# Kernel optimization log

Measured on AMD Instinct MI355X. Metric: run time of the kernel, lower is better.

The kernel has to match this reference:

```python
import jax, jax.numpy as jnp
from jax import lax
import numpy as np

# CenterNet decode config
B, C, H, W = 16, 80, 128, 128  # batch, classes, feature-map H/W (512 input / down_ratio 4)
K = 100                        # top-K detections per image
DOWN = 4.0                     # down_ratio: feature-map coords -> input-image coords


def setup_inputs() -> dict:
    key = jax.random.key(0)
    k1, k2, k3 = jax.random.split(key, 3)
    return {
        "output_heatmap": jax.random.normal(k1, (B, C, H, W), dtype=jnp.float32),
        "output_bbox": jax.random.uniform(k2, (B, 2, H, W), dtype=jnp.float32) * 32.0,  # wh head
        "output_offset": jax.random.uniform(k3, (B, 2, H, W), dtype=jnp.float32),       # sub-pixel offset head
        "image_id": jnp.arange(B, dtype=jnp.int32),
    }


def reference(output_heatmap, output_bbox, output_offset, image_id):
    # 1) peak scores
    hm = jax.nn.sigmoid(output_heatmap)  # [B,C,H,W]
    # 2) 3x3 maxpool NMS: keep only local maxima
    hmax = lax.reduce_window(hm, -jnp.inf, lax.max,
                             window_dimensions=(1, 1, 3, 3),
                             window_strides=(1, 1, 1, 1),
                             padding='SAME')
    hm = jnp.where(hmax == hm, hm, jnp.zeros((), hm.dtype))
    # 3) per-image top-K over all classes and positions
    scores, inds = lax.top_k(hm.reshape(B, C * H * W), K)  # [B,K]
    cls = (inds // (H * W)).astype(jnp.float32)             # [B,K]
    sp = inds % (H * W)                                     # spatial index in [0, H*W)
    ys = (sp // W).astype(jnp.float32)
    xs = (sp % W).astype(jnp.float32)
    # 4) sparse gather of offset and wh at the K peak locations
    off = jnp.take_along_axis(output_offset.reshape(B, 2, H * W), sp[:, None, :], axis=2)  # [B,2,K]
    wh = jnp.take_along_axis(output_bbox.reshape(B, 2, H * W), sp[:, None, :], axis=2)     # [B,2,K]
    cx = xs + off[:, 0]
    cy = ys + off[:, 1]
    w = wh[:, 0]
    h = wh[:, 1]
    # 5) decode to corner boxes in input-image coordinates
    boxes = jnp.stack([cx - w / 2, cy - h / 2, cx + w / 2, cy + h / 2], axis=-1) * DOWN  # [B,K,4]
    img = jnp.broadcast_to(image_id[:, None].astype(jnp.float32), (B, K))
    # detections: [image_id, x1, y1, x2, y2, score, class] -> [B,K,7]
    det = jnp.concatenate([img[..., None], boxes, scores[..., None], cls[..., None]], axis=-1)
    return det
```

## Files before the change

kernel.cpp:

```cpp
#include <hip/hip_runtime.h>

#define BB 16
#define CC 80
#define HWs 16384
#define KK 100
#define NBIN 2048
#define BCAP 2304
#define SBCAP 128

#define OFF_BHIST 0
#define OFF_CUT   131072
#define OFF_PBCNT 131136
#define OFF_PSCNT 136256
#define OFF_REC   141376
#define OFF_SURV  11937856

__device__ __forceinline__ unsigned okey(float f) {
    unsigned u = __float_as_uint(f);
    return (u & 0x80000000u) ? ~u : (u | 0x80000000u);
}

__global__ __launch_bounds__(256) void zero_hist_kernel(int4* __restrict__ bhist) {
    int i = blockIdx.x * 256 + threadIdx.x;
    if (i < BB * NBIN / 4) bhist[i] = make_int4(0, 0, 0, 0);
}

__global__ __launch_bounds__(256) void nms_kernel(const float* __restrict__ hm,
                                                  unsigned* __restrict__ rec,
                                                  int* __restrict__ pbcnt,
                                                  int* __restrict__ bhist) {
    __shared__ int hist[NBIN];
    __shared__ unsigned sbuf[BCAP];
    __shared__ int s_n;
    const int plane = blockIdx.x;
    const int b = plane / CC;
    const int c = plane - b * CC;
    const int t = threadIdx.x;
    const int sx = t & 31;
    const int x0 = sx << 2;
    const int band0 = (t >> 5) << 4;
    const float4* __restrict__ src4 =
        reinterpret_cast<const float4*>(hm + (size_t)plane * HWs);

    for (int i = t; i < NBIN; i += 256) hist[i] = 0;
    if (t == 0) s_n = 0;
    __syncthreads();

    auto hmax3 = [&](const float4& a) -> float4 {
        float vm1 = __shfl_up(a.w, 1, 32);
        float vp4 = __shfl_down(a.x, 1, 32);
        if (sx == 0) vm1 = a.x;
        if (sx == 31) vp4 = a.w;
        float4 h;
        h.x = fmaxf(fmaxf(vm1, a.x), a.y);
        h.y = fmaxf(fmaxf(a.x, a.y), a.z);
        h.z = fmaxf(fmaxf(a.y, a.z), a.w);
        h.w = fmaxf(fmaxf(a.z, a.w), vp4);
        return h;
    };

#pragma unroll
    for (int chunk = 0; chunk < 2; ++chunk) {
        const int y0 = band0 + (chunk << 3);

        float4 w[10];
#pragma unroll
        for (int i = 0; i < 10; ++i) {
            int rr = y0 - 1 + i;
            rr = rr < 0 ? 0 : (rr > 127 ? 127 : rr);
            w[i] = src4[(rr << 5) + sx];
        }
        __builtin_amdgcn_sched_barrier(0);

        float4 hm1 = hmax3(w[0]);
        float4 h0  = hmax3(w[1]);
#pragma unroll
        for (int r = 0; r < 8; ++r) {
            float4 hp1 = hmax3(w[r + 2]);
            float vv[4] = { w[r + 1].x, w[r + 1].y, w[r + 1].z, w[r + 1].w };
            float mm[4] = { fmaxf(fmaxf(hm1.x, h0.x), hp1.x),
                            fmaxf(fmaxf(hm1.y, h0.y), hp1.y),
                            fmaxf(fmaxf(hm1.z, h0.z), hp1.z),
                            fmaxf(fmaxf(hm1.w, h0.w), hp1.w) };
#pragma unroll
            for (int j = 0; j < 4; ++j) {
                if (vv[j] >= mm[j]) {
                    int sl = atomicAdd(&s_n, 1);
                    unsigned bin = okey(vv[j]) >> 21;
                    unsigned idx = ((unsigned)c << 14)
                                 | ((unsigned)(y0 + r) << 7) | (unsigned)(x0 + j);
                    if (sl < BCAP) sbuf[sl] = (bin << 21) | idx;
                }
            }
            hm1 = h0; h0 = hp1;
        }
    }
    __syncthreads();
    int n = s_n; if (n > BCAP) n = BCAP;

    for (int i = t; i < n; i += 256) atomicAdd(&hist[sbuf[i] >> 21], 1);
    __syncthreads();
    for (int i = t; i < NBIN; i += 256) {
        int hv = hist[i];
        if (hv) atomicAdd(&bhist[b * NBIN + i], hv);
    }
    unsigned* __restrict__ rb = rec + (size_t)plane * BCAP;
    for (int i = t; i < n; i += 256) rb[i] = sbuf[i];
    if (t == 0) pbcnt[plane] = n;
}

__global__ __launch_bounds__(256) void cut_kernel(const int* __restrict__ bhist,
                                                  int* __restrict__ cut) {
    __shared__ int csum[256];
    __shared__ int s_cut;
    const int b = blockIdx.x;
    const int t = threadIdx.x;

    int h[8]; int chunk = 0;
#pragma unroll
    for (int j = 0; j < 8; ++j) {
        h[j] = bhist[b * NBIN + (t << 3) + j];
        chunk += h[j];
    }
    csum[t] = chunk;
    if (t == 0) s_cut = 0;
    __syncthreads();
    for (int off = 1; off < 256; off <<= 1) {
        int v = (t + off < 256) ? csum[t + off] : 0;
        __syncthreads();
        csum[t] += v;
        __syncthreads();
    }
    if (csum[0] > KK) {
        int running = (t < 255) ? csum[t + 1] : 0;
        if (csum[t] >= KK && running < KK) {
            for (int j = 7; j >= 0; --j) {
                running += h[j];
                if (running >= KK) { s_cut = (t << 3) + j; break; }
            }
        }
    }
    __syncthreads();
    if (t == 0) cut[b] = s_cut;
}

__global__ __launch_bounds__(256) void filter_kernel(const unsigned* __restrict__ rec,
                                                     const int* __restrict__ pbcnt,
                                                     const int* __restrict__ cut,
                                                     unsigned* __restrict__ surv,
                                                     int* __restrict__ pscnt) {
    __shared__ int s_n;
    const int bx = blockIdx.x;
    const int b = bx / CC;
    const int t = threadIdx.x;
    if (t == 0) s_n = 0;
    __syncthreads();

    int n = pbcnt[bx]; if (n > BCAP) n = BCAP;
    const int cutb = cut[b];
    const unsigned* __restrict__ rb = rec + (size_t)bx * BCAP;
    unsigned* __restrict__ sb = surv + (size_t)bx * SBCAP;
    for (int i = t; i < n; i += 256) {
        unsigned rv = rb[i];
        if ((int)(rv >> 21) >= cutb) {
            int sl = atomicAdd(&s_n, 1);
            if (sl < SBCAP) sb[sl] = rv & 0x1FFFFFu;
        }
    }
    __syncthreads();
    if (t == 0) pscnt[bx] = s_n > SBCAP ? SBCAP : s_n;
}

__global__ __launch_bounds__(256) void topk_kernel(const unsigned* __restrict__ surv,
                                                   const int* __restrict__ pscnt,
                                                   const float* __restrict__ hm,
                                                   const float* __restrict__ bbox,
                                                   const float* __restrict__ offs,
                                                   const int* __restrict__ image_id,
                                                   float* __restrict__ out) {
    __shared__ int lcnt[CC];
    __shared__ unsigned uidx[2048];
    __shared__ unsigned long long list[2048];
    __shared__ int s_n;
    const int b = blockIdx.x;
    const int t = threadIdx.x;
    const float* __restrict__ hb = hm + (size_t)b * CC * HWs;

    if (t < CC) lcnt[t] = pscnt[b * CC + t];
    if (t == 0) s_n = 0;
    __syncthreads();

    for (int s = t; s < CC; s += 256) {
        int cs = lcnt[s]; if (cs > SBCAP) cs = SBCAP;
        if (cs) {
            int base = atomicAdd(&s_n, cs);
            const unsigned* __restrict__ sb = surv + ((size_t)b * CC + s) * SBCAP;
            for (int k = 0; k < cs; ++k)
                if (base + k < 2048) uidx[base + k] = sb[k];
        }
    }
    __syncthreads();
    int n = s_n; if (n > 2048) n = 2048;

    for (int i = t; i < n; i += 256) {
        unsigned idx = uidx[i];
        float lv = hb[idx];
        float s = 1.0f / (1.0f + expf(-lv));
        list[i] = ((unsigned long long)__float_as_uint(s) << 32) | (unsigned)(~idx);
    }
    int P = 128;
    while (P < n) P <<= 1;
    for (int i = n + t; i < P; i += 256) list[i] = 0ull;
    __syncthreads();

    for (int ksz = 2; ksz <= P; ksz <<= 1) {
        for (int j = ksz >> 1; j > 0; j >>= 1) {
            for (int i = t; i < P; i += 256) {
                int ixj = i ^ j;
                if (ixj > i) {
                    unsigned long long a = list[i], bb2 = list[ixj];
                    bool desc = ((i & ksz) == 0);
                    if (desc ? (a < bb2) : (a > bb2)) { list[i] = bb2; list[ixj] = a; }
                }
            }
            __syncthreads();
        }
    }

    if (t < KK) {
        float s = 0.0f; unsigned idx = 0;
        if (t < n) {
            unsigned long long cv = list[t];
            s = __uint_as_float((unsigned)(cv >> 32));
            idx = ~(unsigned)(cv & 0xFFFFFFFFu) & 0x1FFFFFu;
        }
        unsigned sp = idx & (HWs - 1);
        float cls = (float)(idx >> 14);
        float ysf = (float)(sp >> 7);
        float xsf = (float)(sp & 127);
        const float* __restrict__ ob  = offs + (size_t)b * 2 * HWs;
        const float* __restrict__ bbx = bbox + (size_t)b * 2 * HWs;
        float cx = xsf + ob[sp];
        float cy = ysf + ob[HWs + sp];
        float w = bbx[sp];
        float h = bbx[HWs + sp];
        float* row = out + ((size_t)b * KK + t) * 7;
        row[0] = (float)image_id[b];
        row[1] = (cx - w * 0.5f) * 4.0f;
        row[2] = (cy - h * 0.5f) * 4.0f;
        row[3] = (cx + w * 0.5f) * 4.0f;
        row[4] = (cy + h * 0.5f) * 4.0f;
        row[5] = s;
        row[6] = cls;
    }
}

extern "C" void kernel_launch(void* const* d_in, const int* in_sizes, int n_in,
                              void* d_out, int out_size, void* d_ws, size_t ws_size,
                              hipStream_t stream) {
    const float* hm      = (const float*)d_in[0];
    const float* bbox    = (const float*)d_in[1];
    const float* offset  = (const float*)d_in[2];
    const int*   img_id  = (const int*)d_in[3];
    float* out = (float*)d_out;

    char* ws = (char*)d_ws;
    int*      bhist = (int*)(ws + OFF_BHIST);
    int*      cut   = (int*)(ws + OFF_CUT);
    int*      pbcnt = (int*)(ws + OFF_PBCNT);
    int*      pscnt = (int*)(ws + OFF_PSCNT);
    unsigned* rec   = (unsigned*)(ws + OFF_REC);
    unsigned* surv  = (unsigned*)(ws + OFF_SURV);

    zero_hist_kernel<<<32, 256, 0, stream>>>((int4*)bhist);
    nms_kernel<<<BB * CC, 256, 0, stream>>>(hm, rec, pbcnt, bhist);
    cut_kernel<<<BB, 256, 0, stream>>>(bhist, cut);
    filter_kernel<<<BB * CC, 256, 0, stream>>>(rec, pbcnt, cut, surv, pscnt);
    topk_kernel<<<BB, 256, 0, stream>>>(surv, pscnt, hm, bbox, offset, img_id, out);
}
```

Measured before the change: 62.75 us.

## Split NMS planes into half-plane blocks and fold cut computation into filter

Result: faster. 60.34 us (-3.8%).

```diff
diff --git a/kernel.cpp b/kernel.cpp
--- a/kernel.cpp
+++ b/kernel.cpp
@@ -5,15 +5,16 @@
 #define HWs 16384
 #define KK 100
 #define NBIN 2048
-#define BCAP 2304
-#define SBCAP 128
+#define NBLK (BB * CC * 2)
+#define NSLOT 160
+#define BCAP 1152
+#define SBCAP 64
 
 #define OFF_BHIST 0
-#define OFF_CUT   131072
-#define OFF_PBCNT 131136
-#define OFF_PSCNT 136256
-#define OFF_REC   141376
-#define OFF_SURV  11937856
+#define OFF_PBCNT 131072
+#define OFF_PSCNT 141312
+#define OFF_SURV  151552
+#define OFF_REC   806912
 
 __device__ __forceinline__ unsigned okey(float f) {
     unsigned u = __float_as_uint(f);
@@ -32,19 +33,30 @@
     __shared__ int hist[NBIN];
     __shared__ unsigned sbuf[BCAP];
     __shared__ int s_n;
-    const int plane = blockIdx.x;
+    const int blk = blockIdx.x;
+    const int plane = blk >> 1;
+    const int half = blk & 1;
     const int b = plane / CC;
     const int c = plane - b * CC;
     const int t = threadIdx.x;
     const int sx = t & 31;
     const int x0 = sx << 2;
-    const int band0 = (t >> 5) << 4;
+    const int y0 = (half << 6) + ((t >> 5) << 3);
     const float4* __restrict__ src4 =
         reinterpret_cast<const float4*>(hm + (size_t)plane * HWs);
 
     for (int i = t; i < NBIN; i += 256) hist[i] = 0;
     if (t == 0) s_n = 0;
     __syncthreads();
+
+    float4 w[10];
+#pragma unroll
+    for (int i = 0; i < 10; ++i) {
+        int rr = y0 - 1 + i;
+        rr = rr < 0 ? 0 : (rr > 127 ? 127 : rr);
+        w[i] = src4[(rr << 5) + sx];
+    }
+    __builtin_amdgcn_sched_barrier(0);
 
     auto hmax3 = [&](const float4& a) -> float4 {
         float vm1 = __shfl_up(a.w, 1, 32);
@@ -59,41 +71,27 @@
         return h;
     };
 
-#pragma unroll
-    for (int chunk = 0; chunk < 2; ++chunk) {
-        const int y0 = band0 + (chunk << 3);
-
-        float4 w[10];
-#pragma unroll
-        for (int i = 0; i < 10; ++i) {
-            int rr = y0 - 1 + i;
-            rr = rr < 0 ? 0 : (rr > 127 ? 127 : rr);
-            w[i] = src4[(rr << 5) + sx];
-        }
-        __builtin_amdgcn_sched_barrier(0);
-
-        float4 hm1 = hmax3(w[0]);
-        float4 h0  = hmax3(w[1]);
-#pragma unroll
-        for (int r = 0; r < 8; ++r) {
-            float4 hp1 = hmax3(w[r + 2]);
-            float vv[4] = { w[r + 1].x, w[r + 1].y, w[r + 1].z, w[r + 1].w };
-            float mm[4] = { fmaxf(fmaxf(hm1.x, h0.x), hp1.x),
-                            fmaxf(fmaxf(hm1.y, h0.y), hp1.y),
-                            fmaxf(fmaxf(hm1.z, h0.z), hp1.z),
-                            fmaxf(fmaxf(hm1.w, h0.w), hp1.w) };
-#pragma unroll
-            for (int j = 0; j < 4; ++j) {
-                if (vv[j] >= mm[j]) {
-                    int sl = atomicAdd(&s_n, 1);
-                    unsigned bin = okey(vv[j]) >> 21;
-                    unsigned idx = ((unsigned)c << 14)
-                                 | ((unsigned)(y0 + r) << 7) | (unsigned)(x0 + j);
-                    if (sl < BCAP) sbuf[sl] = (bin << 21) | idx;
-                }
+    float4 hm1 = hmax3(w[0]);
+    float4 h0  = hmax3(w[1]);
+#pragma unroll
+    for (int r = 0; r < 8; ++r) {
+        float4 hp1 = hmax3(w[r + 2]);
+        float vv[4] = { w[r + 1].x, w[r + 1].y, w[r + 1].z, w[r + 1].w };
+        float mm[4] = { fmaxf(fmaxf(hm1.x, h0.x), hp1.x),
+                        fmaxf(fmaxf(hm1.y, h0.y), hp1.y),
+                        fmaxf(fmaxf(hm1.z, h0.z), hp1.z),
+                        fmaxf(fmaxf(hm1.w, h0.w), hp1.w) };
+#pragma unroll
+        for (int j = 0; j < 4; ++j) {
+            if (vv[j] >= mm[j]) {
+                int sl = atomicAdd(&s_n, 1);
+                unsigned bin = okey(vv[j]) >> 21;
+                unsigned idx = ((unsigned)c << 14)
+                             | ((unsigned)(y0 + r) << 7) | (unsigned)(x0 + j);
+                if (sl < BCAP) sbuf[sl] = (bin << 21) | idx;
             }
-            hm1 = h0; h0 = hp1;
-        }
+        }
+        hm1 = h0; h0 = hp1;
     }
     __syncthreads();
     int n = s_n; if (n > BCAP) n = BCAP;
@@ -104,16 +102,20 @@
         int hv = hist[i];
         if (hv) atomicAdd(&bhist[b * NBIN + i], hv);
     }
-    unsigned* __restrict__ rb = rec + (size_t)plane * BCAP;
+    unsigned* __restrict__ rb = rec + (size_t)blk * BCAP;
     for (int i = t; i < n; i += 256) rb[i] = sbuf[i];
-    if (t == 0) pbcnt[plane] = n;
-}
-
-__global__ __launch_bounds__(256) void cut_kernel(const int* __restrict__ bhist,
-                                                  int* __restrict__ cut) {
+    if (t == 0) pbcnt[blk] = n;
+}
+
+__global__ __launch_bounds__(256) void filter_kernel(const unsigned* __restrict__ rec,
+                                                     const int* __restrict__ pbcnt,
+                                                     const int* __restrict__ bhist,
+                                                     unsigned* __restrict__ surv,
+                                                     int* __restrict__ pscnt) {
     __shared__ int csum[256];
-    __shared__ int s_cut;
-    const int b = blockIdx.x;
+    __shared__ int s_cut, s_n;
+    const int blk = blockIdx.x;
+    const int b = blk / NSLOT;
     const int t = threadIdx.x;
 
     int h[8]; int chunk = 0;
@@ -123,7 +125,7 @@
         chunk += h[j];
     }
     csum[t] = chunk;
-    if (t == 0) s_cut = 0;
+    if (t == 0) { s_cut = 0; s_n = 0; }
     __syncthreads();
     for (int off = 1; off < 256; off <<= 1) {
         int v = (t + off < 256) ? csum[t + off] : 0;
@@ -141,34 +143,20 @@
         }
     }
     __syncthreads();
-    if (t == 0) cut[b] = s_cut;
-}
-
-__global__ __launch_bounds__(256) void filter_kernel(const unsigned* __restrict__ rec,
-                                                     const int* __restrict__ pbcnt,
-                                                     const int* __restrict__ cut,
-                                                     unsigned* __restrict__ surv,
-                                                     int* __restrict__ pscnt) {
-    __shared__ int s_n;
-    const int bx = blockIdx.x;
-    const int b = bx / CC;
-    const int t = threadIdx.x;
-    if (t == 0) s_n = 0;
-    __syncthreads();
-
-    int n = pbcnt[bx]; if (n > BCAP) n = BCAP;
-    const int cutb = cut[b];
-    const unsigned* __restrict__ rb = rec + (size_t)bx * BCAP;
-    unsigned* __restrict__ sb = surv + (size_t)bx * SBCAP;
+    const unsigned cutb = (unsigned)s_cut;
+
+    int n = pbcnt[blk]; if (n > BCAP) n = BCAP;
+    const unsigned* __restrict__ rb = rec + (size_t)blk * BCAP;
+    unsigned* __restrict__ sb = surv + (size_t)blk * SBCAP;
     for (int i = t; i < n; i += 256) {
         unsigned rv = rb[i];
-        if ((int)(rv >> 21) >= cutb) {
+        if ((rv >> 21) >= cutb) {
             int sl = atomicAdd(&s_n, 1);
             if (sl < SBCAP) sb[sl] = rv & 0x1FFFFFu;
         }
     }
     __syncthreads();
-    if (t == 0) pscnt[bx] = s_n > SBCAP ? SBCAP : s_n;
+    if (t == 0) pscnt[blk] = s_n > SBCAP ? SBCAP : s_n;
 }
 
 __global__ __launch_bounds__(256) void topk_kernel(const unsigned* __restrict__ surv,
@@ -178,7 +166,7 @@
                                                    const float* __restrict__ offs,
                                                    const int* __restrict__ image_id,
                                                    float* __restrict__ out) {
-    __shared__ int lcnt[CC];
+    __shared__ int lcnt[NSLOT];
     __shared__ unsigned uidx[2048];
     __shared__ unsigned long long list[2048];
     __shared__ int s_n;
@@ -186,15 +174,15 @@
     const int t = threadIdx.x;
     const float* __restrict__ hb = hm + (size_t)b * CC * HWs;
 
-    if (t < CC) lcnt[t] = pscnt[b * CC + t];
+    if (t < NSLOT) lcnt[t] = pscnt[b * NSLOT + t];
     if (t == 0) s_n = 0;
     __syncthreads();
 
-    for (int s = t; s < CC; s += 256) {
+    for (int s = t; s < NSLOT; s += 256) {
         int cs = lcnt[s]; if (cs > SBCAP) cs = SBCAP;
         if (cs) {
             int base = atomicAdd(&s_n, cs);
-            const unsigned* __restrict__ sb = surv + ((size_t)b * CC + s) * SBCAP;
+            const unsigned* __restrict__ sb = surv + ((size_t)b * NSLOT + s) * SBCAP;
             for (int k = 0; k < cs; ++k)
                 if (base + k < 2048) uidx[base + k] = sb[k];
         }
@@ -266,15 +254,13 @@
 
     char* ws = (char*)d_ws;
     int*      bhist = (int*)(ws + OFF_BHIST);
-    int*      cut   = (int*)(ws + OFF_CUT);
     int*      pbcnt = (int*)(ws + OFF_PBCNT);
     int*      pscnt = (int*)(ws + OFF_PSCNT);
+    unsigned* surv  = (unsigned*)(ws + OFF_SURV);
     unsigned* rec   = (unsigned*)(ws + OFF_REC);
-    unsigned* surv  = (unsigned*)(ws + OFF_SURV);
 
     zero_hist_kernel<<<32, 256, 0, stream>>>((int4*)bhist);
-    nms_kernel<<<BB * CC, 256, 0, stream>>>(hm, rec, pbcnt, bhist);
-    cut_kernel<<<BB, 256, 0, stream>>>(bhist, cut);
-    filter_kernel<<<BB * CC, 256, 0, stream>>>(rec, pbcnt, cut, surv, pscnt);
+    nms_kernel<<<NBLK, 256, 0, stream>>>(hm, rec, pbcnt, bhist);
+    filter_kernel<<<NBLK, 256, 0, stream>>>(rec, pbcnt, bhist, surv, pscnt);
     topk_kernel<<<BB, 256, 0, stream>>>(surv, pscnt, hm, bbox, offset, img_id, out);
 }
```
